# Kernel tuning notes

Measured on AMD Instinct MI355X. Metric: run time of the kernel, lower is better.

The kernel has to match this reference:

```python
import jax, jax.numpy as jnp
import numpy as np

B, T, N_EMBD, HEAD_SIZE = 4, 4096, 32, 32


def setup_inputs() -> dict:
    key = jax.random.key(0)
    k1, k2, k3, k4 = jax.random.split(key, 4)
    x = jax.random.normal(k1, (B, T, N_EMBD), dtype=jnp.float32)
    Wq = jax.random.normal(k2, (HEAD_SIZE, N_EMBD), dtype=jnp.float32) * (N_EMBD ** -0.5)
    Wk = jax.random.normal(k3, (HEAD_SIZE, N_EMBD), dtype=jnp.float32) * (N_EMBD ** -0.5)
    Wv = jax.random.normal(k4, (HEAD_SIZE, N_EMBD), dtype=jnp.float32) * (N_EMBD ** -0.5)
    return {"x": x, "Wq": Wq, "Wk": Wk, "Wv": Wv}


def reference(x, Wq, Wk, Wv):
    # Linear(bias=False): y = x @ W.T  -> [B, T, head_size]
    q = jnp.einsum('btn,hn->bth', x, Wq)
    k = jnp.einsum('btn,hn->bth', x, Wk)
    v = jnp.einsum('btn,hn->bth', x, Wv)
    scale = q.shape[-1] ** -0.5
    # [B, T, T] attention scores
    wei = jnp.einsum('bth,bsh->bts', q, k) * scale
    # Faithful to source: tril the scores, then mask entries equal to 0
    tril = jnp.tril(wei)
    wei = jax.nn.softmax(jnp.where(tril == 0, -jnp.inf, tril), axis=-1)
    return jnp.einsum('bts,bsh->bth', wei, v)
```

## Files before the change

kernel.cpp:

```cpp
#include <hip/hip_runtime.h>
#include <cmath>

#define BB 4
#define TT 4096
#define NE 32
#define HS 32

#define IPB2 1088
#define MAXSP 16
#define SLOT 288
#define FNEG (-1.0e30f)
#define BIAS 6.0f
#define SC2  0.25506953149031156f

typedef unsigned int uint32;
typedef __fp16 half2v __attribute__((ext_vector_type(2)));
typedef __fp16 half4v __attribute__((ext_vector_type(4)));
typedef __fp16 half8v __attribute__((ext_vector_type(8)));
typedef float f32x4 __attribute__((ext_vector_type(4)));

__device__ __forceinline__ half2v u2h(uint32 u) {
    union { uint32 u; half2v h; } x; x.u = u; return x.h;
}

#if __has_builtin(__builtin_amdgcn_cvt_pkrtz)
__device__ __forceinline__ half2v pkf16(float a, float b) {
    return __builtin_amdgcn_cvt_pkrtz(a, b);
}
#else
__device__ __forceinline__ half2v pkf16(float a, float b) {
    half2v h; h.x = (__fp16)a; h.y = (__fp16)b; return h;
}
#endif

__global__ __launch_bounds__(256) void qkv_proj(
    const float* __restrict__ x,
    const float* __restrict__ Wq,
    const float* __restrict__ Wk,
    const float* __restrict__ Wv,
    __fp16* __restrict__ Qh, __fp16* __restrict__ Kh,
    __fp16* __restrict__ Vt8)
{
    int tid = blockIdx.x * 256 + threadIdx.x;
    int row = tid >> 5;
    int h   = tid & 31;
    const float4* xr4 = reinterpret_cast<const float4*>(x + (size_t)row * NE);
    float4 xv4[8];
    #pragma unroll
    for (int k = 0; k < 8; ++k) xv4[k] = xr4[k];
    const float* xv = (const float*)xv4;
    float aq = 0.f, ak = 0.f, av = 0.f;
    #pragma unroll
    for (int d = 0; d < NE; ++d) {
        aq = fmaf(xv[d], Wq[h * NE + d], aq);
        ak = fmaf(xv[d], Wk[h * NE + d], ak);
        av = fmaf(xv[d], Wv[h * NE + d], av);
    }
    size_t o = (size_t)row * HS + h;
    Qh[o] = (__fp16)(aq * SC2);
    Kh[o] = (__fp16)ak;
    int b = row >> 12, t = row & (TT - 1);
    Vt8[((size_t)(b * (TT / 4) + (t >> 2)) * 16 + (h & 15)) * 8
        + (h >> 4) * 4 + (t & 3)] = (__fp16)av;
}

__global__ __launch_bounds__(256, 4) void attn_partial(
    const __fp16* __restrict__ Qh, const __fp16* __restrict__ Kh,
    const __fp16* __restrict__ Vt8, float* __restrict__ part)
{
    int wave = threadIdx.x >> 6;
    int lane = threadIdx.x & 63;
    int item = blockIdx.x * 4 + wave;
    int b = item / IPB2;
    int r = item - b * IPB2;
    int g = (int)((sqrtf((float)(1 + r)) - 1.0f) * 0.5f);
    if (g < 0) g = 0;
    while (4 * (g + 1) * (g + 2) <= r) ++g;
    while (4 * g * (g + 1) > r) --g;
    int rr = r - 4 * g * (g + 1);
    int tq = rr / (g + 1);
    int tt = 8 * g + tq;
    int sp = rr - tq * (g + 1);
    int qt0 = tt * 32;
    int kbase = sp * 256;
    int kend  = min(kbase + 256, qt0 + 32);
    int nsub  = (kend - kbase) >> 4;
    bool hasdiag = (kend == qt0 + 32);
    int nfast = nsub - (hasdiag ? 2 : 0);

    int c = lane & 15;
    int q = lane >> 4;

    const __fp16* Qb = Qh  + (size_t)b * TT * HS;
    const __fp16* Kb = Kh  + (size_t)b * TT * HS;
    const __fp16* Vb = Vt8 + (size_t)b * (TT / 4) * 128;

    union U4H8  { uint4 u; half8v h; };
    union U4H44 { uint4 u; half4v h4[2]; };
    union H4    { half4v h4; half2v h2[2]; };
    union H4U4  { half2v h[4]; uint4 u; };

    U4H8 qf0; qf0.u = *(const uint4*)(Qb + (size_t)(qt0 + c) * HS + 8 * q);
    U4H8 qf1; qf1.u = *(const uint4*)(Qb + (size_t)(qt0 + 16 + c) * HS + 8 * q);

    const f32x4 cbias = {-BIAS, -BIAS, -BIAS, -BIAS};
    float l0 = 0.f, l1 = 0.f;
    f32x4 o00 = {0.f,0.f,0.f,0.f}, o01 = o00, o10 = o00, o11 = o00;

    auto dofast = [&](int kb) {
        U4H8 kf; kf.u = *(const uint4*)(Kb + (size_t)(kb + c) * HS + 8 * q);
        U4H44 vf; vf.u = *(const uint4*)(Vb + (size_t)((kb >> 2) + q) * 128 + c * 8);
        f32x4 s0 = __builtin_amdgcn_mfma_f32_16x16x32_f16(kf.h, qf0.h, cbias, 0, 0, 0);
        f32x4 s1 = __builtin_amdgcn_mfma_f32_16x16x32_f16(kf.h, qf1.h, cbias, 0, 0, 0);
        float p0[4], p1[4];
        #pragma unroll
        for (int j = 0; j < 4; ++j) {
            p0[j] = exp2f((s0[j] != -BIAS) ? s0[j] : FNEG);
            p1[j] = exp2f((s1[j] != -BIAS) ? s1[j] : FNEG);
        }
        l0 += (p0[0] + p0[1]) + (p0[2] + p0[3]);
        l1 += (p1[0] + p1[1]) + (p1[2] + p1[3]);
        H4 pf0; pf0.h2[0] = pkf16(p0[0], p0[1]); pf0.h2[1] = pkf16(p0[2], p0[3]);
        H4 pf1; pf1.h2[0] = pkf16(p1[0], p1[1]); pf1.h2[1] = pkf16(p1[2], p1[3]);
        o00 = __builtin_amdgcn_mfma_f32_16x16x16f16(vf.h4[0], pf0.h4, o00, 0, 0, 0);
        o01 = __builtin_amdgcn_mfma_f32_16x16x16f16(vf.h4[1], pf0.h4, o01, 0, 0, 0);
        o10 = __builtin_amdgcn_mfma_f32_16x16x16f16(vf.h4[0], pf1.h4, o10, 0, 0, 0);
        o11 = __builtin_amdgcn_mfma_f32_16x16x16f16(vf.h4[1], pf1.h4, o11, 0, 0, 0);
    };

    auto domask = [&](int kb) {
        U4H8 kf; kf.u = *(const uint4*)(Kb + (size_t)(kb + c) * HS + 8 * q);
        U4H44 vf; vf.u = *(const uint4*)(Vb + (size_t)((kb >> 2) + q) * 128 + c * 8);
        f32x4 s0 = __builtin_amdgcn_mfma_f32_16x16x32_f16(kf.h, qf0.h, cbias, 0, 0, 0);
        f32x4 s1 = __builtin_amdgcn_mfma_f32_16x16x32_f16(kf.h, qf1.h, cbias, 0, 0, 0);
        int r0 = kb - qt0 + 4 * q;
        int r1 = r0 - 16;
        float p0[4], p1[4];
        #pragma unroll
        for (int j = 0; j < 4; ++j) {
            float w0 = (s0[j] != -BIAS) ? s0[j] : FNEG;
            float w1 = (s1[j] != -BIAS) ? s1[j] : FNEG;
            if (r0 + j > c) w0 = FNEG;
            if (r1 + j > c) w1 = FNEG;
            p0[j] = exp2f(w0);
            p1[j] = exp2f(w1);
        }
        l0 += (p0[0] + p0[1]) + (p0[2] + p0[3]);
        l1 += (p1[0] + p1[1]) + (p1[2] + p1[3]);
        H4 pf0; pf0.h2[0] = pkf16(p0[0], p0[1]); pf0.h2[1] = pkf16(p0[2], p0[3]);
        H4 pf1; pf1.h2[0] = pkf16(p1[0], p1[1]); pf1.h2[1] = pkf16(p1[2], p1[3]);
        o00 = __builtin_amdgcn_mfma_f32_16x16x16f16(vf.h4[0], pf0.h4, o00, 0, 0, 0);
        o01 = __builtin_amdgcn_mfma_f32_16x16x16f16(vf.h4[1], pf0.h4, o01, 0, 0, 0);
        o10 = __builtin_amdgcn_mfma_f32_16x16x16f16(vf.h4[0], pf1.h4, o10, 0, 0, 0);
        o11 = __builtin_amdgcn_mfma_f32_16x16x16f16(vf.h4[1], pf1.h4, o11, 0, 0, 0);
    };

    int kb = kbase;
    #pragma unroll 2
    for (int i = 0; i < nfast; ++i) { dofast(kb); kb += 16; }
    if (hasdiag) { domask(kb); domask(kb + 16); }

    float lt0 = l0 + __shfl_xor(l0, 16); lt0 += __shfl_xor(lt0, 32);
    float lt1 = l1 + __shfl_xor(l1, 16); lt1 += __shfl_xor(lt1, 32);

    float* P0 = part + (size_t)((b * 256 + 2 * tt) * MAXSP + sp) * SLOT;
    float* P1 = P0 + (size_t)MAXSP * SLOT;
    if (q == 0) { P0[16 + c] = lt0; P1[16 + c] = lt1; }
    H4U4 a;
    a.h[0] = pkf16(o00[0], o00[1]); a.h[1] = pkf16(o00[2], o00[3]);
    a.h[2] = pkf16(o01[0], o01[1]); a.h[3] = pkf16(o01[2], o01[3]);
    *((uint4*)((uint32*)(P0 + 32) + c * 16 + q * 4)) = a.u;
    a.h[0] = pkf16(o10[0], o10[1]); a.h[1] = pkf16(o10[2], o10[3]);
    a.h[2] = pkf16(o11[0], o11[1]); a.h[3] = pkf16(o11[2], o11[3]);
    *((uint4*)((uint32*)(P1 + 32) + c * 16 + q * 4)) = a.u;
}

__global__ __launch_bounds__(256) void attn_combine(
    const float* __restrict__ part, float* __restrict__ out)
{
    int tid = blockIdx.x * 256 + threadIdx.x;
    int hq = tid & 3;
    int c  = (tid >> 2) & 15;
    int t  = (tid >> 6) & 255;
    int b  = tid >> 14;
    int ns = (t >> 4) + 1;

    const float* base = part + (size_t)(b * 256 + t) * MAXSP * SLOT;

    float acc[8];
    #pragma unroll
    for (int k = 0; k < 8; ++k) acc[k] = 0.f;
    float L = 0.f;
    for (int s = 0; s < ns; ++s) {
        const float* P = base + (size_t)s * SLOT;
        L += P[16 + c];
        uint4 ov = *(const uint4*)((const uint32*)(P + 32) + c * 16 + 4 * hq);
        const uint32* ovp = (const uint32*)&ov;
        #pragma unroll
        for (int pr = 0; pr < 4; ++pr) {
            half2v hh = u2h(ovp[pr]);
            acc[2 * pr]     += (float)hh.x;
            acc[2 * pr + 1] += (float)hh.y;
        }
    }
    float invL = 1.0f / L;
    float* orow = out + ((size_t)(b * TT + t * 16 + c)) * HS;
    float4 w0 = {acc[0] * invL, acc[1] * invL, acc[2] * invL, acc[3] * invL};
    float4 w1 = {acc[4] * invL, acc[5] * invL, acc[6] * invL, acc[7] * invL};
    *(float4*)(orow + 4 * hq) = w0;
    *(float4*)(orow + 16 + 4 * hq) = w1;
}

extern "C" void kernel_launch(void* const* d_in, const int* in_sizes, int n_in,
                              void* d_out, int out_size, void* d_ws, size_t ws_size,
                              hipStream_t stream)
{
    const float* x  = (const float*)d_in[0];
    const float* Wq = (const float*)d_in[1];
    const float* Wk = (const float*)d_in[2];
    const float* Wv = (const float*)d_in[3];
    float* out = (float*)d_out;

    __fp16* Qh  = (__fp16*)d_ws;
    __fp16* Kh  = Qh + (size_t)BB * TT * HS;
    __fp16* Vt8 = Kh + (size_t)BB * TT * HS;
    float* part = (float*)(Vt8 + (size_t)BB * TT * HS);

    qkv_proj<<<dim3((BB * TT * HS) / 256), dim3(256), 0, stream>>>(
        x, Wq, Wk, Wv, Qh, Kh, Vt8);
    attn_partial<<<dim3((BB * IPB2) / 4), dim3(256), 0, stream>>>(
        Qh, Kh, Vt8, part);
    attn_combine<<<dim3(256), dim3(256), 0, stream>>>(part, out);
}
```

Measured before the change: 113.0 us.

## Fuse split-K combine into attention kernel via last-arriver atomic counter

Removes the separate combine kernel launch. Each wave of the partial-attention kernel atomically increments a per-tile counter after writing its partial result, and the last wave for that query tile reduces all partials and writes the normalized output. Counters are zeroed in the projection kernel. This saves one launch and its tail, in exchange for atomics, fences and a serialized reduction tail inside the last-arriving wave.

```diff
diff --git a/kernel.cpp b/kernel.cpp
--- a/kernel.cpp
+++ b/kernel.cpp
@@ -39,8 +39,13 @@
     const float* __restrict__ Wk,
     const float* __restrict__ Wv,
     __fp16* __restrict__ Qh, __fp16* __restrict__ Kh,
-    __fp16* __restrict__ Vt8)
+    __fp16* __restrict__ Vt8, uint32* __restrict__ cnt)
 {
+    if (blockIdx.x == 0) {
+        cnt[threadIdx.x] = 0;
+        cnt[256 + threadIdx.x] = 0;
+    }
+
     int tid = blockIdx.x * 256 + threadIdx.x;
     int row = tid >> 5;
     int h   = tid & 31;
@@ -66,7 +71,8 @@
 
 __global__ __launch_bounds__(256, 4) void attn_partial(
     const __fp16* __restrict__ Qh, const __fp16* __restrict__ Kh,
-    const __fp16* __restrict__ Vt8, float* __restrict__ part)
+    const __fp16* __restrict__ Vt8, float* __restrict__ part,
+    uint32* __restrict__ cnt, float* __restrict__ out)
 {
     int wave = threadIdx.x >> 6;
     int lane = threadIdx.x & 63;
@@ -173,42 +179,47 @@
     a.h[0] = pkf16(o10[0], o10[1]); a.h[1] = pkf16(o10[2], o10[3]);
     a.h[2] = pkf16(o11[0], o11[1]); a.h[3] = pkf16(o11[2], o11[3]);
     *((uint4*)((uint32*)(P1 + 32) + c * 16 + q * 4)) = a.u;
-}
-
-__global__ __launch_bounds__(256) void attn_combine(
-    const float* __restrict__ part, float* __restrict__ out)
-{
-    int tid = blockIdx.x * 256 + threadIdx.x;
-    int hq = tid & 3;
-    int c  = (tid >> 2) & 15;
-    int t  = (tid >> 6) & 255;
-    int b  = tid >> 14;
-    int ns = (t >> 4) + 1;
-
-    const float* base = part + (size_t)(b * 256 + t) * MAXSP * SLOT;
-
-    float acc[8];
+
+    __threadfence();
+    uint32 old = 0;
+    if (lane == 0)
+        old = __hip_atomic_fetch_add(&cnt[b * 128 + tt], 1u,
+                                     __ATOMIC_RELAXED,
+                                     __HIP_MEMORY_SCOPE_AGENT);
+    old = __shfl((int)old, 0);
+    if (old != (uint32)g) return;
+    __threadfence();
+
+    int ns = g + 1;
+    int hq = lane & 3;
+    int cc = lane >> 2;
     #pragma unroll
-    for (int k = 0; k < 8; ++k) acc[k] = 0.f;
-    float L = 0.f;
-    for (int s = 0; s < ns; ++s) {
-        const float* P = base + (size_t)s * SLOT;
-        L += P[16 + c];
-        uint4 ov = *(const uint4*)((const uint32*)(P + 32) + c * 16 + 4 * hq);
-        const uint32* ovp = (const uint32*)&ov;
+    for (int hf = 0; hf < 2; ++hf) {
+        int t16 = 2 * tt + hf;
+        const float* base = part + (size_t)((b * 256 + t16) * MAXSP) * SLOT;
+        float acc[8];
         #pragma unroll
-        for (int pr = 0; pr < 4; ++pr) {
-            half2v hh = u2h(ovp[pr]);
-            acc[2 * pr]     += (float)hh.x;
-            acc[2 * pr + 1] += (float)hh.y;
+        for (int k2 = 0; k2 < 8; ++k2) acc[k2] = 0.f;
+        float L = 0.f;
+        for (int s = 0; s < ns; ++s) {
+            const float* P = base + (size_t)s * SLOT;
+            L += P[16 + cc];
+            uint4 ov = *(const uint4*)((const uint32*)(P + 32) + cc * 16 + 4 * hq);
+            const uint32* ovp = (const uint32*)&ov;
+            #pragma unroll
+            for (int pr = 0; pr < 4; ++pr) {
+                half2v hh = u2h(ovp[pr]);
+                acc[2 * pr]     += (float)hh.x;
+                acc[2 * pr + 1] += (float)hh.y;
+            }
         }
+        float invL = 1.0f / L;
+        float* orow = out + ((size_t)(b * TT + t16 * 16 + cc)) * HS;
+        float4 w0 = {acc[0] * invL, acc[1] * invL, acc[2] * invL, acc[3] * invL};
+        float4 w1 = {acc[4] * invL, acc[5] * invL, acc[6] * invL, acc[7] * invL};
+        *(float4*)(orow + 4 * hq) = w0;
+        *(float4*)(orow + 16 + 4 * hq) = w1;
     }
-    float invL = 1.0f / L;
-    float* orow = out + ((size_t)(b * TT + t * 16 + c)) * HS;
-    float4 w0 = {acc[0] * invL, acc[1] * invL, acc[2] * invL, acc[3] * invL};
-    float4 w1 = {acc[4] * invL, acc[5] * invL, acc[6] * invL, acc[7] * invL};
-    *(float4*)(orow + 4 * hq) = w0;
-    *(float4*)(orow + 16 + 4 * hq) = w1;
 }
 
 extern "C" void kernel_launch(void* const* d_in, const int* in_sizes, int n_in,
@@ -225,10 +236,10 @@
     __fp16* Kh  = Qh + (size_t)BB * TT * HS;
     __fp16* Vt8 = Kh + (size_t)BB * TT * HS;
     float* part = (float*)(Vt8 + (size_t)BB * TT * HS);
+    uint32* cnt = (uint32*)(part + (size_t)BB * 256 * MAXSP * SLOT);
 
     qkv_proj<<<dim3((BB * TT * HS) / 256), dim3(256), 0, stream>>>(
-        x, Wq, Wk, Wv, Qh, Kh, Vt8);
+        x, Wq, Wk, Wv, Qh, Kh, Vt8, cnt);
     attn_partial<<<dim3((BB * IPB2) / 4), dim3(256), 0, stream>>>(
-        Qh, Kh, Vt8, part);
-    attn_combine<<<dim3(256), dim3(256), 0, stream>>>(part, out);
-}
+        Qh, Kh, Vt8, part, cnt, out);
+}
```

After: 239.4 us. 112% more time.
